# Performance work log

Hardware: AMD Instinct MI355X
Metric: run time of the kernel (lower is better)

The kernel has to match this reference:

```python
import jax, jax.numpy as jnp
import numpy as np

B, S, D = 2, 2048, 2048
H = 16
NOPE, ROPE, VDIM = 128, 64, 128
QKD = NOPE + ROPE  # 192
KV_RANK = 512
EPS = 1e-6
SCALE = QKD ** -0.5  # rope_factor <= 1.0 -> no mscale correction


def _rotate_half(x):
    h = x.shape[-1] // 2
    return jnp.concatenate([-x[..., h:], x[..., :h]], axis=-1)


def _rms_norm(x, w):
    var = jnp.mean(jnp.square(x), axis=-1, keepdims=True)
    return x * jax.lax.rsqrt(var + EPS) * w


def setup_inputs() -> dict:
    key = jax.random.key(0)
    ks = jax.random.split(key, 8)
    hidden_states = jax.random.normal(ks[0], (B, S, D), dtype=jnp.float32)
    cos = jax.random.uniform(ks[1], (S, ROPE), dtype=jnp.float32)
    sin = jax.random.uniform(ks[2], (S, ROPE), dtype=jnp.float32)
    # parameters (torch Linear stores [out, in]; keep same layout)
    wq_w = jax.random.normal(ks[3], (H * QKD, D), dtype=jnp.float32) * (D ** -0.5)
    wkv_a_w = jax.random.normal(ks[4], (KV_RANK + ROPE, D), dtype=jnp.float32) * (D ** -0.5)
    kv_norm_w = jnp.ones((KV_RANK,), dtype=jnp.float32)
    wkv_b_w = jax.random.normal(ks[5], (H * (NOPE + VDIM), KV_RANK), dtype=jnp.float32) * (KV_RANK ** -0.5)
    wo_w = jax.random.normal(ks[6], (D, H * VDIM), dtype=jnp.float32) * ((H * VDIM) ** -0.5)
    return dict(hidden_states=hidden_states, cos=cos, sin=sin,
                wq_w=wq_w, wkv_a_w=wkv_a_w, kv_norm_w=kv_norm_w,
                wkv_b_w=wkv_b_w, wo_w=wo_w)


def reference(hidden_states, cos, sin, wq_w, wkv_a_w, kv_norm_w, wkv_b_w, wo_w):
    x = hidden_states
    # q projection (q_lora_rank == 0 path)
    q = jnp.einsum('bsd,od->bso', x, wq_w).reshape(B, S, H, QKD)
    q_nope, q_pe = q[..., :NOPE], q[..., NOPE:]
    # low-rank kv
    kv_all = jnp.einsum('bsd,od->bso', x, wkv_a_w)  # [B,S,KV_RANK+ROPE]
    kv, k_pe = kv_all[..., :KV_RANK], kv_all[..., KV_RANK:]
    kv_proj = jnp.einsum('bsr,or->bso', _rms_norm(kv, kv_norm_w), wkv_b_w)
    kv_proj = kv_proj.reshape(B, S, H, NOPE + VDIM)
    k_nope, v = kv_proj[..., :NOPE], kv_proj[..., NOPE:]
    # rotary on pe parts; k_pe broadcast over heads
    c = cos[None, :, None, :]  # [1,S,1,ROPE]
    s = sin[None, :, None, :]
    q_pe = q_pe * c + _rotate_half(q_pe) * s
    k_pe_h = k_pe[:, :, None, :]  # broadcast over heads
    k_pe_h = k_pe_h * c + _rotate_half(k_pe_h) * s
    k_pe_h = jnp.broadcast_to(k_pe_h, (B, S, H, ROPE))
    k = jnp.concatenate([k_nope, k_pe_h], axis=-1)  # [B,S,H,QKD]
    qf = jnp.concatenate([q_nope, q_pe], axis=-1)
    # naive attention, fp32 softmax
    scores = jnp.einsum('bshd,bthd->bsht', qf, k) * SCALE
    attn = jax.nn.softmax(scores.astype(jnp.float32), axis=-1).astype(x.dtype)
    out = jnp.einsum('bsht,bthd->bshd', attn, v).reshape(B, S, H * VDIM)
    return jnp.einsum('bsf,of->bso', out, wo_w)
```

## Files before the change

kernel.cpp:

```cpp
#include <hip/hip_runtime.h>
#include <cstdint>


typedef _Float16 f16;
typedef _Float16 f16x8 __attribute__((ext_vector_type(8)));
typedef _Float16 f16x4 __attribute__((ext_vector_type(4)));
typedef float    f32x4 __attribute__((ext_vector_type(4)));

#define SCALE 0.07216878364870322f

__device__ __forceinline__ void gl2lds16(const void* g, void* lds_wave_base) {
  __builtin_amdgcn_global_load_lds(
      (const __attribute__((address_space(1))) uint32_t*)(uintptr_t)g,
      (__attribute__((address_space(3))) uint32_t*)(uint32_t)(uintptr_t)lds_wave_base,
      16, 0, 0);
}

__global__ __launch_bounds__(256) void k_cvt(
    const float* __restrict__ x, const float* __restrict__ wq,
    const float* __restrict__ wkvb, const float* __restrict__ wo,
    const float* __restrict__ wkva,
    f16* __restrict__ xb, f16* __restrict__ wqb,
    f16* __restrict__ wkvbb, f16* __restrict__ wob,
    f16* __restrict__ wkvab)
{
  size_t i = ((size_t)blockIdx.x * 256 + threadIdx.x) * 4;
  if (i >= 20971520ull) {
    size_t il = i - 20971520ull;
    int r = (int)(il >> 11);
    f16x4 h;
    if (r < 576) {
      float4 v = *(const float4*)(wkva + il);
      h[0]=(f16)v.x; h[1]=(f16)v.y; h[2]=(f16)v.z; h[3]=(f16)v.w;
    } else { h[0]=h[1]=h[2]=h[3]=(f16)0.f; }
    *(f16x4*)(wkvab + il) = h;
    return;
  }
  const float* src; f16* dst; size_t off; float scl = 1.0f;
  if (i < 8388608ull)            { src = x;    dst = xb;    off = i; }
  else if (i < 14680064ull)      { src = wq;   dst = wqb;   off = i - 8388608ull; scl = SCALE; }
  else if (i < 16777216ull)      { src = wkvb; dst = wkvbb; off = i - 14680064ull; }
  else                           { src = wo;   dst = wob;   off = i - 16777216ull; }
  float4 v = *(const float4*)(src + off);
  f16x4 h; h[0]=(f16)(v.x*scl); h[1]=(f16)(v.y*scl); h[2]=(f16)(v.z*scl); h[3]=(f16)(v.w*scl);
  *(f16x4*)(dst + off) = h;
}

template<class Epi>
__device__ __forceinline__ void gemm_core(const f16* __restrict__ Ablk,
                                          const f16* __restrict__ Bblk,
                                          int K, Epi epi)
{
  __shared__ __align__(16) f16 As[128 * 64];
  __shared__ __align__(16) f16 Bs[128 * 64];

  const int tid  = threadIdx.x;
  const int lane = tid & 63;
  const int wv   = tid >> 6;
  const int wm = (wv >> 1) * 64, wn = (wv & 1) * 64;
  const int lrow = lane & 15;
  const int lk   = lane >> 4;

  f32x4 acc[4][4];
#pragma unroll
  for (int i = 0; i < 4; ++i)
#pragma unroll
    for (int j = 0; j < 4; ++j) acc[i][j] = f32x4{0.f, 0.f, 0.f, 0.f};

  for (int k0 = 0; k0 < K; k0 += 64) {
    __syncthreads();
#pragma unroll
    for (int it = 0; it < 4; ++it) {
      int s  = it * 256 + tid;
      int r  = s >> 3, sc = s & 7;
      int gc = sc ^ (r & 7);
      gl2lds16(Ablk + (size_t)r * K + k0 + gc * 8, (f16*)As + (size_t)(it * 256 + wv * 64) * 8);
      gl2lds16(Bblk + (size_t)r * K + k0 + gc * 8, (f16*)Bs + (size_t)(it * 256 + wv * 64) * 8);
    }
    __syncthreads();

#pragma unroll
    for (int ks = 0; ks < 2; ++ks) {
      f16x8 af[4], bf[4];
#pragma unroll
      for (int i = 0; i < 4; ++i) {
        int ra = wm + i * 16 + lrow;
        int ca = (ks * 4 + lk) ^ (ra & 7);
        af[i] = *(const f16x8*)(As + ra * 64 + ca * 8);
        int rb = wn + i * 16 + lrow;
        int cb = (ks * 4 + lk) ^ (rb & 7);
        bf[i] = *(const f16x8*)(Bs + rb * 64 + cb * 8);
      }
#pragma unroll
      for (int i = 0; i < 4; ++i)
#pragma unroll
        for (int j = 0; j < 4; ++j)
          acc[i][j] = __builtin_amdgcn_mfma_f32_16x16x32_f16(af[i], bf[j], acc[i][j], 0, 0, 0);
    }
  }
  epi(acc, wm, wn, lk, lrow);
}

__global__ __launch_bounds__(256, 3) void k_gemm_qkva(
    const f16* __restrict__ xb, const f16* __restrict__ wqb,
    const f16* __restrict__ wkvab, const float* __restrict__ cosb,
    const float* __restrict__ sinb,
    f16* __restrict__ qraw, f16* __restrict__ kva)
{
  int nb = blockIdx.x, m0 = blockIdx.y * 128;
  bool isq = nb < 24;
  const f16* Bblk; f16* Cb; int ldc;
  if (isq) { Bblk = wqb + (size_t)nb * 128 * 2048;
             Cb = qraw + (size_t)m0 * 3072 + nb * 128; ldc = 3072; }
  else     { int n0 = (nb - 24) * 128;
             Bblk = wkvab + (size_t)n0 * 2048;
             Cb = kva + (size_t)m0 * 640 + n0; ldc = 640; }
  gemm_core(xb + (size_t)m0 * 2048, Bblk, 2048,
    [&](f32x4 (&acc)[4][4], int wm, int wn, int lk, int lrow) {
      if (isq && (((nb << 1) + (wn >> 6)) % 3) == 2) {
#pragma unroll
        for (int i = 0; i < 4; ++i)
#pragma unroll
          for (int rr = 0; rr < 4; ++rr) {
            int row = wm + i * 16 + lk * 4 + rr;
            int s = (m0 + row) & 2047;
            const float* cbp = cosb + (size_t)s * 64;
            const float* sbp = sinb + (size_t)s * 64;
#pragma unroll
            for (int j = 0; j < 4; ++j) {
              int t = j * 16 + lrow;
              float v  = acc[i][j][rr];
              float pr = acc[i][j ^ 2][rr];
              float o = (j < 2) ? (v * cbp[t] - pr * sbp[t])
                                : (v * cbp[t] + pr * sbp[t]);
              Cb[(size_t)row * ldc + wn + j * 16 + lrow] = (f16)o;
            }
          }
        return;
      }
#pragma unroll
      for (int i = 0; i < 4; ++i)
#pragma unroll
        for (int rr = 0; rr < 4; ++rr) {
          int row = wm + i * 16 + lk * 4 + rr;
#pragma unroll
          for (int j = 0; j < 4; ++j)
            Cb[(size_t)row * ldc + wn + j * 16 + lrow] = (f16)acc[i][j][rr];
        }
    });
}

__global__ __launch_bounds__(256, 3) void k_gemm_kvb(
    const f16* __restrict__ kvn, const f16* __restrict__ wkvbb,
    f16* __restrict__ knope, f16* __restrict__ vf)
{
  int nb = blockIdx.x, m0 = blockIdx.y * 128;
  int hh = nb >> 1;
  bool isv = nb & 1;
  gemm_core(kvn + (size_t)m0 * 512, wkvbb + (size_t)nb * 128 * 512, 512,
    [&](f32x4 (&acc)[4][4], int wm, int wn, int lk, int lrow) {
      if (isv) {
#pragma unroll
        for (int i = 0; i < 4; ++i)
#pragma unroll
          for (int j = 0; j < 4; ++j) {
            int vd = wn + j * 16 + lrow;
            int trow = m0 + wm + i * 16 + lk * 4;
            int bb = trow >> 11, ss = trow & 2047;
            f16x4 pk;
#pragma unroll
            for (int rr = 0; rr < 4; ++rr) pk[rr] = (f16)acc[i][j][rr];
            *(f16x4*)(vf + ((size_t)(bb * 16 + hh) * 128 + vd) * 2048 + ss) = pk;
          }
      } else {
#pragma unroll
        for (int i = 0; i < 4; ++i)
#pragma unroll
          for (int rr = 0; rr < 4; ++rr) {
            int trow = m0 + wm + i * 16 + lk * 4 + rr;
#pragma unroll
            for (int j = 0; j < 4; ++j)
              knope[(size_t)trow * 2048 + hh * 128 + wn + j * 16 + lrow] = (f16)acc[i][j][rr];
          }
      }
    });
}

__global__ __launch_bounds__(256, 3) void k_gemm_out(
    const f16* __restrict__ aout, const f16* __restrict__ wob, float* __restrict__ out)
{
  int n0 = blockIdx.x * 128, m0 = blockIdx.y * 128;
  gemm_core(aout + (size_t)m0 * 2048, wob + (size_t)n0 * 2048, 2048,
    [&](f32x4 (&acc)[4][4], int wm, int wn, int lk, int lrow) {
#pragma unroll
      for (int i = 0; i < 4; ++i)
#pragma unroll
        for (int rr = 0; rr < 4; ++rr) {
          int row = m0 + wm + i * 16 + lk * 4 + rr;
#pragma unroll
          for (int j = 0; j < 4; ++j)
            out[(size_t)row * 2048 + n0 + wn + j * 16 + lrow] = acc[i][j][rr];
        }
    });
}

__global__ __launch_bounds__(256) void k_rmsnorm_rope(
    const f16* __restrict__ kva, const float* __restrict__ w,
    const float* __restrict__ cosb, const float* __restrict__ sinb,
    f16* __restrict__ kvn, f16* __restrict__ kper)
{
  int row = blockIdx.x;
  int s = row & 2047;
  const f16* in = kva + (size_t)row * 640;
  int t = threadIdx.x;
  float v0 = (float)in[t], v1 = (float)in[t + 256];
  float ss = v0 * v0 + v1 * v1;
#pragma unroll
  for (int m = 1; m < 64; m <<= 1) ss += __shfl_xor(ss, m);
  __shared__ float red[4];
  if ((t & 63) == 0) red[t >> 6] = ss;
  __syncthreads();
  float tot = red[0] + red[1] + red[2] + red[3];
  float sc = rsqrtf(tot * (1.0f / 512.0f) + 1e-6f);
  kvn[(size_t)row * 512 + t]       = (f16)(v0 * sc * w[t]);
  kvn[(size_t)row * 512 + t + 256] = (f16)(v1 * sc * w[t + 256]);
  if (t < 32) {
    float a = (float)in[512 + t], bq = (float)in[512 + t + 32];
    float c0 = cosb[s * 64 + t], s0 = sinb[s * 64 + t];
    float c1 = cosb[s * 64 + t + 32], s1 = sinb[s * 64 + t + 32];
    kper[(size_t)row * 64 + t]      = (f16)(a * c0 - bq * s0);
    kper[(size_t)row * 64 + t + 32] = (f16)(bq * c1 + a * s1);
  }
}

#define PSTR 84

__global__ __launch_bounds__(512, 2) void k_attn(
    const f16* __restrict__ qraw, const f16* __restrict__ knope,
    const f16* __restrict__ kper, const f16* __restrict__ vf,
    f16* __restrict__ aout)
{
  int linear = blockIdx.x;
  int xcd  = linear & 7;
  int slot = linear >> 3;
  int hb   = (xcd << 2) | (slot & 3);
  int qt   = slot >> 2;
  int h = hb & 15, b = hb >> 4;
  int q0 = qt * 256;
  int tid = threadIdx.x, lane = tid & 63, wv = tid >> 6;
  int lrow = lane & 15, lk = lane >> 4;

  __shared__ __align__(16) f16 Ks[2][64 * 192];
  __shared__ __align__(16) f16 Vs[2][128 * 64];
  __shared__ __align__(16) f16 Ps[8][32 * PSTR];

  f16x8 qfr[2][6];
#pragma unroll
  for (int m = 0; m < 2; ++m) {
    const f16* qb = qraw + ((size_t)(b * 2048 + q0 + wv * 32 + m * 16 + lrow)) * 3072
                    + h * 192 + lk * 8;
#pragma unroll
    for (int ks = 0; ks < 6; ++ks) qfr[m][ks] = *(const f16x8*)(qb + ks * 32);
  }

  f32x4 oacc[2][8];
#pragma unroll
  for (int m = 0; m < 2; ++m)
#pragma unroll
    for (int i = 0; i < 8; ++i) oacc[m][i] = f32x4{0.f, 0.f, 0.f, 0.f};
  float l_st[2][4];
#pragma unroll
  for (int m = 0; m < 2; ++m)
#pragma unroll
    for (int r = 0; r < 4; ++r) l_st[m][r] = 0.f;

  const f16* knb = knope + ((size_t)b * 2048) * 2048 + h * 128;
  const f16* kpb = kper + (size_t)b * 2048 * 64;
  const f16* vb_ = vf + ((size_t)(b * 16 + h)) * 128 * 2048;

  const char* kp_ptr[3]; int kp_step[3];
#pragma unroll
  for (int it = 0; it < 3; ++it) {
    int s = it * 512 + tid;
    int r = s / 24, c = s - r * 24;
    int gc = c ^ (r & 7);
    if (gc < 16) { kp_ptr[it] = (const char*)(knb + (size_t)r * 2048 + gc * 8); kp_step[it] = 64 * 2048 * 2; }
    else         { kp_ptr[it] = (const char*)(kpb + (size_t)r * 64 + (gc - 16) * 8); kp_step[it] = 64 * 64 * 2; }
  }
  const char* vp_ptr[2];
#pragma unroll
  for (int it = 0; it < 2; ++it) {
    int s = it * 512 + tid;
    int r = s >> 3, c = s & 7, gc = c ^ (r & 7);
    vp_ptr[it] = (const char*)(vb_ + (size_t)r * 2048 + gc * 8);
  }

#pragma unroll
  for (int it = 0; it < 3; ++it) {
    gl2lds16(kp_ptr[it], (f16*)Ks[0] + (size_t)(it * 512 + wv * 64) * 8);
    kp_ptr[it] += kp_step[it];
  }
#pragma unroll
  for (int it = 0; it < 2; ++it) {
    gl2lds16(vp_ptr[it], (f16*)Vs[0] + (size_t)(it * 512 + wv * 64) * 8);
    vp_ptr[it] += 64 * 2;
  }

  int cur = 0;
  for (int t0 = 0; t0 < 2048; t0 += 64) {
    __syncthreads();
    if (t0 + 64 < 2048) {
#pragma unroll
      for (int it = 0; it < 3; ++it) {
        gl2lds16(kp_ptr[it], (f16*)Ks[cur ^ 1] + (size_t)(it * 512 + wv * 64) * 8);
        kp_ptr[it] += kp_step[it];
      }
#pragma unroll
      for (int it = 0; it < 2; ++it) {
        gl2lds16(vp_ptr[it], (f16*)Vs[cur ^ 1] + (size_t)(it * 512 + wv * 64) * 8);
        vp_ptr[it] += 64 * 2;
      }
    }
    const f16* Kc = Ks[cur];
    const f16* Vc = Vs[cur];

    f32x4 sacc[2][4];
#pragma unroll
    for (int m = 0; m < 2; ++m)
#pragma unroll
      for (int nt = 0; nt < 4; ++nt) sacc[m][nt] = f32x4{0.f, 0.f, 0.f, 0.f};
    __builtin_amdgcn_s_setprio(1);
#pragma unroll
    for (int nt = 0; nt < 4; ++nt) {
      int rb = nt * 16 + lrow;
#pragma unroll
      for (int ks = 0; ks < 6; ++ks) {
        int cc = (ks * 4 + lk) ^ (rb & 7);
        f16x8 bfr = *(const f16x8*)(Kc + rb * 192 + cc * 8);
        sacc[0][nt] = __builtin_amdgcn_mfma_f32_16x16x32_f16(qfr[0][ks], bfr, sacc[0][nt], 0, 0, 0);
        sacc[1][nt] = __builtin_amdgcn_mfma_f32_16x16x32_f16(qfr[1][ks], bfr, sacc[1][nt], 0, 0, 0);
      }
    }
    __builtin_amdgcn_s_setprio(0);

#pragma unroll
    for (int m = 0; m < 2; ++m) {
#pragma unroll
      for (int r = 0; r < 4; ++r) {
        float p0 = __expf(sacc[m][0][r]);
        float p1 = __expf(sacc[m][1][r]);
        float p2 = __expf(sacc[m][2][r]);
        float p3 = __expf(sacc[m][3][r]);
        l_st[m][r] += (p0 + p1) + (p2 + p3);
        int prow = (m * 16 + lk * 4 + r) * PSTR;
        Ps[wv][prow + 0 * 16 + lrow] = (f16)p0;
        Ps[wv][prow + 1 * 16 + lrow] = (f16)p1;
        Ps[wv][prow + 2 * 16 + lrow] = (f16)p2;
        Ps[wv][prow + 3 * 16 + lrow] = (f16)p3;
      }
    }
    __builtin_amdgcn_s_waitcnt(0xC07F);

    __builtin_amdgcn_s_setprio(1);
#pragma unroll
    for (int ks2 = 0; ks2 < 2; ++ks2) {
      f16x8 pa0 = *(const f16x8*)(&Ps[wv][(0 * 16 + lrow) * PSTR + ks2 * 32 + lk * 8]);
      f16x8 pa1 = *(const f16x8*)(&Ps[wv][(1 * 16 + lrow) * PSTR + ks2 * 32 + lk * 8]);
#pragma unroll
      for (int nv = 0; nv < 8; ++nv) {
        int rv = nv * 16 + lrow;
        int cc = (ks2 * 4 + lk) ^ (rv & 7);
        f16x8 vbf = *(const f16x8*)(Vc + rv * 64 + cc * 8);
        oacc[0][nv] = __builtin_amdgcn_mfma_f32_16x16x32_f16(pa0, vbf, oacc[0][nv], 0, 0, 0);
        oacc[1][nv] = __builtin_amdgcn_mfma_f32_16x16x32_f16(pa1, vbf, oacc[1][nv], 0, 0, 0);
      }
    }
    __builtin_amdgcn_s_setprio(0);
    cur ^= 1;
  }

  float rinv[2][4];
#pragma unroll
  for (int m = 0; m < 2; ++m)
#pragma unroll
    for (int r = 0; r < 4; ++r) {
      float l = l_st[m][r];
#pragma unroll
      for (int msk = 1; msk < 16; msk <<= 1) l += __shfl_xor(l, msk);
      rinv[m][r] = 1.0f / l;
    }
#pragma unroll
  for (int m = 0; m < 2; ++m) {
    f16* ob = aout + ((size_t)(b * 2048 + q0 + wv * 32 + m * 16 + lk * 4)) * 2048
              + h * 128 + lrow;
#pragma unroll
    for (int nv = 0; nv < 8; ++nv)
#pragma unroll
      for (int rr = 0; rr < 4; ++rr)
        ob[(size_t)rr * 2048 + nv * 16] = (f16)(oacc[m][nv][rr] * rinv[m][rr]);
  }
}

extern "C" void kernel_launch(void* const* d_in, const int* in_sizes, int n_in,
                              void* d_out, int out_size, void* d_ws, size_t ws_size,
                              hipStream_t stream)
{
  const float* x    = (const float*)d_in[0];
  const float* cosb = (const float*)d_in[1];
  const float* sinb = (const float*)d_in[2];
  const float* wq   = (const float*)d_in[3];
  const float* wkva = (const float*)d_in[4];
  const float* knw  = (const float*)d_in[5];
  const float* wkvb = (const float*)d_in[6];
  const float* wo   = (const float*)d_in[7];
  float* out = (float*)d_out;

  char* p = (char*)d_ws;
  auto take = [&](size_t elems) { char* r = p; p += (elems * 2 + 255) & ~(size_t)255; return r; };
  f16* xb    = (f16*)take(8388608ull);
  f16* wqb   = (f16*)take(6291456ull);
  f16* wkvab = (f16*)take(1310720ull);
  f16* wkvbb = (f16*)take(2097152ull);
  f16* wob   = (f16*)take(4194304ull);
  f16* qraw  = (f16*)take(12582912ull);
  f16* kva   = (f16*)take(2621440ull);
  f16* kvn   = (f16*)take(2097152ull);
  f16* kper  = (f16*)take(262144ull);
  f16* knope = (f16*)take(8388608ull);
  f16* vf    = (f16*)take(8388608ull);
  f16* aout  = (f16*)take(8388608ull);

  k_cvt<<<21760, 256, 0, stream>>>(x, wq, wkvb, wo, wkva, xb, wqb, wkvbb, wob, wkvab);
  k_gemm_qkva<<<dim3(29, 32), 256, 0, stream>>>(xb, wqb, wkvab, cosb, sinb, qraw, kva);
  k_rmsnorm_rope<<<4096, 256, 0, stream>>>(kva, knw, cosb, sinb, kvn, kper);
  k_gemm_kvb<<<dim3(32, 32), 256, 0, stream>>>(kvn, wkvbb, knope, vf);
  k_attn<<<dim3(256), 512, 0, stream>>>(qraw, knope, kper, vf, aout);
  k_gemm_out<<<dim3(16, 32), 256, 0, stream>>>(aout, wob, out);
}
```

Measured before the change: 389.9 us.

## Halve attention Q and KV tiles, double the grid, fold log2e into Q scale

The attention kernel now gives each wave 16 query rows instead of 32 and streams K/V in 32-key tiles instead of 64. This doubles the grid to 512 blocks and raises the launch-bounds occupancy target to 4 blocks per CU, trading register and LDS footprint for more resident waves to hide latency. The price is that each K/V tile is reused by half as many queries, so global and L2 traffic for K/V roughly doubles. Separately, log2(e) is folded into the Q weight scale at conversion so the softmax can use the hardware exp2 instead of __expf.

```diff
diff --git a/kernel.cpp b/kernel.cpp
--- a/kernel.cpp
+++ b/kernel.cpp
@@ -7,7 +7,7 @@
 typedef _Float16 f16x4 __attribute__((ext_vector_type(4)));
 typedef float    f32x4 __attribute__((ext_vector_type(4)));
 
-#define SCALE 0.07216878364870322f
+#define SCALE_L2E 0.104117550f
 
 __device__ __forceinline__ void gl2lds16(const void* g, void* lds_wave_base) {
   __builtin_amdgcn_global_load_lds(
@@ -38,7 +38,7 @@
   }
   const float* src; f16* dst; size_t off; float scl = 1.0f;
   if (i < 8388608ull)            { src = x;    dst = xb;    off = i; }
-  else if (i < 14680064ull)      { src = wq;   dst = wqb;   off = i - 8388608ull; scl = SCALE; }
+  else if (i < 14680064ull)      { src = wq;   dst = wqb;   off = i - 8388608ull; scl = SCALE_L2E; }
   else if (i < 16777216ull)      { src = wkvb; dst = wkvbb; off = i - 14680064ull; }
   else                           { src = wo;   dst = wob;   off = i - 16777216ull; }
   float4 v = *(const float4*)(src + off);
@@ -233,9 +233,9 @@
   }
 }
 
-#define PSTR 84
-
-__global__ __launch_bounds__(512, 2) void k_attn(
+#define PSTR 42
+
+__global__ __launch_bounds__(512, 4) void k_attn(
     const f16* __restrict__ qraw, const f16* __restrict__ knope,
     const f16* __restrict__ kper, const f16* __restrict__ vf,
     f16* __restrict__ aout)
@@ -246,159 +246,125 @@
   int hb   = (xcd << 2) | (slot & 3);
   int qt   = slot >> 2;
   int h = hb & 15, b = hb >> 4;
-  int q0 = qt * 256;
+  int q0 = qt * 128;
   int tid = threadIdx.x, lane = tid & 63, wv = tid >> 6;
   int lrow = lane & 15, lk = lane >> 4;
 
-  __shared__ __align__(16) f16 Ks[2][64 * 192];
-  __shared__ __align__(16) f16 Vs[2][128 * 64];
-  __shared__ __align__(16) f16 Ps[8][32 * PSTR];
-
-  f16x8 qfr[2][6];
-#pragma unroll
-  for (int m = 0; m < 2; ++m) {
-    const f16* qb = qraw + ((size_t)(b * 2048 + q0 + wv * 32 + m * 16 + lrow)) * 3072
+  __shared__ __align__(16) f16 Ks[2][32 * 192];
+  __shared__ __align__(16) f16 Vs[2][128 * 32];
+  __shared__ __align__(16) f16 Ps[8][16 * PSTR];
+
+  f16x8 qfr[6];
+  {
+    const f16* qb = qraw + ((size_t)(b * 2048 + q0 + wv * 16 + lrow)) * 3072
                     + h * 192 + lk * 8;
 #pragma unroll
-    for (int ks = 0; ks < 6; ++ks) qfr[m][ks] = *(const f16x8*)(qb + ks * 32);
-  }
-
-  f32x4 oacc[2][8];
-#pragma unroll
-  for (int m = 0; m < 2; ++m)
-#pragma unroll
-    for (int i = 0; i < 8; ++i) oacc[m][i] = f32x4{0.f, 0.f, 0.f, 0.f};
-  float l_st[2][4];
-#pragma unroll
-  for (int m = 0; m < 2; ++m)
-#pragma unroll
-    for (int r = 0; r < 4; ++r) l_st[m][r] = 0.f;
+    for (int ks = 0; ks < 6; ++ks) qfr[ks] = *(const f16x8*)(qb + ks * 32);
+  }
+
+  f32x4 oacc[8];
+#pragma unroll
+  for (int i = 0; i < 8; ++i) oacc[i] = f32x4{0.f, 0.f, 0.f, 0.f};
+  float l_st[4];
+#pragma unroll
+  for (int r = 0; r < 4; ++r) l_st[r] = 0.f;
 
   const f16* knb = knope + ((size_t)b * 2048) * 2048 + h * 128;
   const f16* kpb = kper + (size_t)b * 2048 * 64;
   const f16* vb_ = vf + ((size_t)(b * 16 + h)) * 128 * 2048;
 
-  const char* kp_ptr[3]; int kp_step[3];
-#pragma unroll
-  for (int it = 0; it < 3; ++it) {
+  const char* kp_ptr[2]; int kp_step[2];
+#pragma unroll
+  for (int it = 0; it < 2; ++it) {
     int s = it * 512 + tid;
     int r = s / 24, c = s - r * 24;
     int gc = c ^ (r & 7);
-    if (gc < 16) { kp_ptr[it] = (const char*)(knb + (size_t)r * 2048 + gc * 8); kp_step[it] = 64 * 2048 * 2; }
-    else         { kp_ptr[it] = (const char*)(kpb + (size_t)r * 64 + (gc - 16) * 8); kp_step[it] = 64 * 64 * 2; }
-  }
-  const char* vp_ptr[2];
-#pragma unroll
-  for (int it = 0; it < 2; ++it) {
-    int s = it * 512 + tid;
-    int r = s >> 3, c = s & 7, gc = c ^ (r & 7);
-    vp_ptr[it] = (const char*)(vb_ + (size_t)r * 2048 + gc * 8);
-  }
-
-#pragma unroll
-  for (int it = 0; it < 3; ++it) {
-    gl2lds16(kp_ptr[it], (f16*)Ks[0] + (size_t)(it * 512 + wv * 64) * 8);
-    kp_ptr[it] += kp_step[it];
-  }
-#pragma unroll
-  for (int it = 0; it < 2; ++it) {
-    gl2lds16(vp_ptr[it], (f16*)Vs[0] + (size_t)(it * 512 + wv * 64) * 8);
-    vp_ptr[it] += 64 * 2;
-  }
+    if (gc < 16) { kp_ptr[it] = (const char*)(knb + (size_t)r * 2048 + gc * 8); kp_step[it] = 32 * 2048 * 2; }
+    else         { kp_ptr[it] = (const char*)(kpb + (size_t)r * 64 + (gc - 16) * 8); kp_step[it] = 32 * 64 * 2; }
+  }
+  const char* vp_ptr;
+  {
+    int r = tid >> 2, c = tid & 3;
+    int gc = c ^ ((r ^ (r >> 2)) & 3);
+    vp_ptr = (const char*)(vb_ + (size_t)r * 2048 + gc * 8);
+  }
+
+  gl2lds16(kp_ptr[0], (f16*)Ks[0] + (size_t)(wv * 64) * 8);
+  kp_ptr[0] += kp_step[0];
+  if (wv < 4) gl2lds16(kp_ptr[1], (f16*)Ks[0] + (size_t)(512 + wv * 64) * 8);
+  kp_ptr[1] += kp_step[1];
+  gl2lds16(vp_ptr, (f16*)Vs[0] + (size_t)(wv * 64) * 8);
+  vp_ptr += 32 * 2;
 
   int cur = 0;
-  for (int t0 = 0; t0 < 2048; t0 += 64) {
+  for (int t0 = 0; t0 < 2048; t0 += 32) {
     __syncthreads();
-    if (t0 + 64 < 2048) {
-#pragma unroll
-      for (int it = 0; it < 3; ++it) {
-        gl2lds16(kp_ptr[it], (f16*)Ks[cur ^ 1] + (size_t)(it * 512 + wv * 64) * 8);
-        kp_ptr[it] += kp_step[it];
-      }
-#pragma unroll
-      for (int it = 0; it < 2; ++it) {
-        gl2lds16(vp_ptr[it], (f16*)Vs[cur ^ 1] + (size_t)(it * 512 + wv * 64) * 8);
-        vp_ptr[it] += 64 * 2;
-      }
+    if (t0 + 32 < 2048) {
+      gl2lds16(kp_ptr[0], (f16*)Ks[cur ^ 1] + (size_t)(wv * 64) * 8);
+      kp_ptr[0] += kp_step[0];
+      if (wv < 4) gl2lds16(kp_ptr[1], (f16*)Ks[cur ^ 1] + (size_t)(512 + wv * 64) * 8);
+      kp_ptr[1] += kp_step[1];
+      gl2lds16(vp_ptr, (f16*)Vs[cur ^ 1] + (size_t)(wv * 64) * 8);
+      vp_ptr += 32 * 2;
     }
     const f16* Kc = Ks[cur];
     const f16* Vc = Vs[cur];
 
-    f32x4 sacc[2][4];
-#pragma unroll
-    for (int m = 0; m < 2; ++m)
-#pragma unroll
-      for (int nt = 0; nt < 4; ++nt) sacc[m][nt] = f32x4{0.f, 0.f, 0.f, 0.f};
+    f32x4 sacc[2];
+    sacc[0] = f32x4{0.f, 0.f, 0.f, 0.f};
+    sacc[1] = f32x4{0.f, 0.f, 0.f, 0.f};
     __builtin_amdgcn_s_setprio(1);
 #pragma unroll
-    for (int nt = 0; nt < 4; ++nt) {
+    for (int nt = 0; nt < 2; ++nt) {
       int rb = nt * 16 + lrow;
 #pragma unroll
       for (int ks = 0; ks < 6; ++ks) {
         int cc = (ks * 4 + lk) ^ (rb & 7);
         f16x8 bfr = *(const f16x8*)(Kc + rb * 192 + cc * 8);
-        sacc[0][nt] = __builtin_amdgcn_mfma_f32_16x16x32_f16(qfr[0][ks], bfr, sacc[0][nt], 0, 0, 0);
-        sacc[1][nt] = __builtin_amdgcn_mfma_f32_16x16x32_f16(qfr[1][ks], bfr, sacc[1][nt], 0, 0, 0);
+        sacc[nt] = __builtin_amdgcn_mfma_f32_16x16x32_f16(qfr[ks], bfr, sacc[nt], 0, 0, 0);
       }
     }
     __builtin_amdgcn_s_setprio(0);
 
 #pragma unroll
-    for (int m = 0; m < 2; ++m) {
-#pragma unroll
-      for (int r = 0; r < 4; ++r) {
-        float p0 = __expf(sacc[m][0][r]);
-        float p1 = __expf(sacc[m][1][r]);
-        float p2 = __expf(sacc[m][2][r]);
-        float p3 = __expf(sacc[m][3][r]);
-        l_st[m][r] += (p0 + p1) + (p2 + p3);
-        int prow = (m * 16 + lk * 4 + r) * PSTR;
-        Ps[wv][prow + 0 * 16 + lrow] = (f16)p0;
-        Ps[wv][prow + 1 * 16 + lrow] = (f16)p1;
-        Ps[wv][prow + 2 * 16 + lrow] = (f16)p2;
-        Ps[wv][prow + 3 * 16 + lrow] = (f16)p3;
-      }
+    for (int r = 0; r < 4; ++r) {
+      float p0 = __builtin_amdgcn_exp2f(sacc[0][r]);
+      float p1 = __builtin_amdgcn_exp2f(sacc[1][r]);
+      l_st[r] += p0 + p1;
+      int prow = (lk * 4 + r) * PSTR;
+      Ps[wv][prow + lrow]      = (f16)p0;
+      Ps[wv][prow + 16 + lrow] = (f16)p1;
     }
     __builtin_amdgcn_s_waitcnt(0xC07F);
 
     __builtin_amdgcn_s_setprio(1);
-#pragma unroll
-    for (int ks2 = 0; ks2 < 2; ++ks2) {
-      f16x8 pa0 = *(const f16x8*)(&Ps[wv][(0 * 16 + lrow) * PSTR + ks2 * 32 + lk * 8]);
-      f16x8 pa1 = *(const f16x8*)(&Ps[wv][(1 * 16 + lrow) * PSTR + ks2 * 32 + lk * 8]);
-#pragma unroll
-      for (int nv = 0; nv < 8; ++nv) {
-        int rv = nv * 16 + lrow;
-        int cc = (ks2 * 4 + lk) ^ (rv & 7);
-        f16x8 vbf = *(const f16x8*)(Vc + rv * 64 + cc * 8);
-        oacc[0][nv] = __builtin_amdgcn_mfma_f32_16x16x32_f16(pa0, vbf, oacc[0][nv], 0, 0, 0);
-        oacc[1][nv] = __builtin_amdgcn_mfma_f32_16x16x32_f16(pa1, vbf, oacc[1][nv], 0, 0, 0);
-      }
+    f16x8 pa = *(const f16x8*)(&Ps[wv][lrow * PSTR + lk * 8]);
+#pragma unroll
+    for (int nv = 0; nv < 8; ++nv) {
+      int rv = nv * 16 + lrow;
+      int cc = lk ^ ((rv ^ (rv >> 2)) & 3);
+      f16x8 vbf = *(const f16x8*)(Vc + rv * 32 + cc * 8);
+      oacc[nv] = __builtin_amdgcn_mfma_f32_16x16x32_f16(pa, vbf, oacc[nv], 0, 0, 0);
     }
     __builtin_amdgcn_s_setprio(0);
     cur ^= 1;
   }
 
-  float rinv[2][4];
-#pragma unroll
-  for (int m = 0; m < 2; ++m)
-#pragma unroll
-    for (int r = 0; r < 4; ++r) {
-      float l = l_st[m][r];
-#pragma unroll
-      for (int msk = 1; msk < 16; msk <<= 1) l += __shfl_xor(l, msk);
-      rinv[m][r] = 1.0f / l;
-    }
-#pragma unroll
-  for (int m = 0; m < 2; ++m) {
-    f16* ob = aout + ((size_t)(b * 2048 + q0 + wv * 32 + m * 16 + lk * 4)) * 2048
-              + h * 128 + lrow;
-#pragma unroll
-    for (int nv = 0; nv < 8; ++nv)
-#pragma unroll
-      for (int rr = 0; rr < 4; ++rr)
-        ob[(size_t)rr * 2048 + nv * 16] = (f16)(oacc[m][nv][rr] * rinv[m][rr]);
-  }
+  float rinv[4];
+#pragma unroll
+  for (int r = 0; r < 4; ++r) {
+    float l = l_st[r];
+#pragma unroll
+    for (int msk = 1; msk < 16; msk <<= 1) l += __shfl_xor(l, msk);
+    rinv[r] = 1.0f / l;
+  }
+  f16* ob = aout + ((size_t)(b * 2048 + q0 + wv * 16 + lk * 4)) * 2048
+            + h * 128 + lrow;
+#pragma unroll
+  for (int nv = 0; nv < 8; ++nv)
+#pragma unroll
+    for (int rr = 0; rr < 4; ++rr)
+      ob[(size_t)rr * 2048 + nv * 16] = (f16)(oacc[nv][rr] * rinv[rr]);
 }
 
 extern "C" void kernel_launch(void* const* d_in, const int* in_sizes, int n_in,
@@ -434,6 +400,6 @@
   k_gemm_qkva<<<dim3(29, 32), 256, 0, stream>>>(xb, wqb, wkvab, cosb, sinb, qraw, kva);
   k_rmsnorm_rope<<<4096, 256, 0, stream>>>(kva, knw, cosb, sinb, kvn, kper);
   k_gemm_kvb<<<dim3(32, 32), 256, 0, stream>>>(kvn, wkvbb, knope, vf);
-  k_attn<<<dim3(256), 512, 0, stream>>>(qraw, knope, kper, vf, aout);
+  k_attn<<<dim3(512), 512, 0, stream>>>(qraw, knope, kper, vf, aout);
   k_gemm_out<<<dim3(16, 32), 256, 0, stream>>>(aout, wob, out);
 }
```

After: 385.5 us. No clear change (-1.1%).

## Use 256x256 double-buffered GEMM tiles and fold log2e into Q scale

Applied to the files above, without the earlier changes.

Adds a 256x256 tile GEMM core with 512 threads and double-buffered LDS, prefetching the next K-tile while MFMAs run. The QKV-A and KV-B projections move to this core, which raises data reuse per block and cuts the number of blocks. The softmax scale now includes log2(e), so attention can use the native exp2 instead of expf. Risks: the grids get smaller (240 and 256 blocks), so load balance across CUs is worse; the 128 KB of LDS limits occupancy; and the padded wkva rows add wasted work.

```diff
diff --git a/kernel.cpp b/kernel.cpp
--- a/kernel.cpp
+++ b/kernel.cpp
@@ -7,7 +7,7 @@
 typedef _Float16 f16x4 __attribute__((ext_vector_type(4)));
 typedef float    f32x4 __attribute__((ext_vector_type(4)));
 
-#define SCALE 0.07216878364870322f
+#define SCALE_L2E 0.104117550f
 
 __device__ __forceinline__ void gl2lds16(const void* g, void* lds_wave_base) {
   __builtin_amdgcn_global_load_lds(
@@ -38,12 +38,202 @@
   }
   const float* src; f16* dst; size_t off; float scl = 1.0f;
   if (i < 8388608ull)            { src = x;    dst = xb;    off = i; }
-  else if (i < 14680064ull)      { src = wq;   dst = wqb;   off = i - 8388608ull; scl = SCALE; }
+  else if (i < 14680064ull)      { src = wq;   dst = wqb;   off = i - 8388608ull; scl = SCALE_L2E; }
   else if (i < 16777216ull)      { src = wkvb; dst = wkvbb; off = i - 14680064ull; }
   else                           { src = wo;   dst = wob;   off = i - 16777216ull; }
   float4 v = *(const float4*)(src + off);
   f16x4 h; h[0]=(f16)(v.x*scl); h[1]=(f16)(v.y*scl); h[2]=(f16)(v.z*scl); h[3]=(f16)(v.w*scl);
   *(f16x4*)(dst + off) = h;
+}
+
+template<class Epi>
+__device__ __forceinline__ void gemm256_core(const f16* __restrict__ Ablk,
+                                             const f16* __restrict__ Bblk,
+                                             int K, Epi epi)
+{
+  __shared__ __align__(16) f16 As[2][256 * 64];
+  __shared__ __align__(16) f16 Bs[2][256 * 64];
+
+  const int tid  = threadIdx.x;
+  const int lane = tid & 63;
+  const int wv   = tid >> 6;
+  const int wm   = (wv >> 2) * 128;
+  const int wn   = (wv & 3) * 64;
+  const int lrow = lane & 15;
+  const int lk   = lane >> 4;
+
+  f32x4 acc[8][4];
+#pragma unroll
+  for (int i = 0; i < 8; ++i)
+#pragma unroll
+    for (int j = 0; j < 4; ++j) acc[i][j] = f32x4{0.f, 0.f, 0.f, 0.f};
+
+  const int NT = K >> 6;
+
+  const f16* aptr[4]; const f16* bptr[4]; int ldsbase[4];
+#pragma unroll
+  for (int q = 0; q < 4; ++q) {
+    int s = q * 512 + tid;
+    int r = s >> 3, c = s & 7;
+    int gc = c ^ (r & 7);
+    aptr[q] = Ablk + (size_t)r * K + gc * 8;
+    bptr[q] = Bblk + (size_t)r * K + gc * 8;
+    ldsbase[q] = (q * 512 + wv * 64) * 8;
+  }
+
+#pragma unroll
+  for (int q = 0; q < 4; ++q) gl2lds16(aptr[q], (f16*)As[0] + ldsbase[q]);
+#pragma unroll
+  for (int q = 0; q < 4; ++q) gl2lds16(bptr[q], (f16*)Bs[0] + ldsbase[q]);
+
+  for (int t = 0; t < NT; ++t) {
+    const int cur = t & 1;
+    asm volatile("s_waitcnt vmcnt(0)" ::: "memory");
+    __builtin_amdgcn_s_barrier();
+    asm volatile("" ::: "memory");
+    const f16* Ac = As[cur];
+    const f16* Bc = Bs[cur];
+    const bool more = (t + 1 < NT);
+    const int koff = (t + 1) * 64;
+#pragma unroll
+    for (int p = 0; p < 4; ++p) {
+      if (p == 0 && more) {
+#pragma unroll
+        for (int q = 0; q < 4; ++q)
+          gl2lds16(aptr[q] + koff, (f16*)As[cur ^ 1] + ldsbase[q]);
+      }
+      if (p == 1 && more) {
+#pragma unroll
+        for (int q = 0; q < 4; ++q)
+          gl2lds16(bptr[q] + koff, (f16*)Bs[cur ^ 1] + ldsbase[q]);
+      }
+      const int mh = p >> 1, nh = p & 1;
+      f16x8 af[2][4], bf[2][2];
+#pragma unroll
+      for (int ks = 0; ks < 2; ++ks) {
+#pragma unroll
+        for (int i = 0; i < 4; ++i) {
+          int ra = wm + mh * 64 + i * 16 + lrow;
+          int ca = (ks * 4 + lk) ^ (ra & 7);
+          af[ks][i] = *(const f16x8*)(Ac + ra * 64 + ca * 8);
+        }
+#pragma unroll
+        for (int j = 0; j < 2; ++j) {
+          int rb = wn + nh * 32 + j * 16 + lrow;
+          int cb = (ks * 4 + lk) ^ (rb & 7);
+          bf[ks][j] = *(const f16x8*)(Bc + rb * 64 + cb * 8);
+        }
+      }
+      __builtin_amdgcn_s_setprio(1);
+#pragma unroll
+      for (int ks = 0; ks < 2; ++ks)
+#pragma unroll
+        for (int i = 0; i < 4; ++i)
+#pragma unroll
+          for (int j = 0; j < 2; ++j)
+            acc[mh * 4 + i][nh * 2 + j] = __builtin_amdgcn_mfma_f32_16x16x32_f16(
+                af[ks][i], bf[ks][j], acc[mh * 4 + i][nh * 2 + j], 0, 0, 0);
+      __builtin_amdgcn_s_setprio(0);
+    }
+  }
+  epi(acc, wm, wn, lk, lrow);
+}
+
+__global__ __launch_bounds__(512, 2) void k_gemm_qkva(
+    const f16* __restrict__ xb, const f16* __restrict__ wqb,
+    const f16* __restrict__ wkvab, const float* __restrict__ cosb,
+    const float* __restrict__ sinb,
+    f16* __restrict__ qraw, f16* __restrict__ kva)
+{
+  int nb = blockIdx.x, m0 = blockIdx.y * 256;
+  bool isq = nb < 12;
+  const f16* Bblk = isq ? wqb + (size_t)nb * 256 * 2048
+                        : wkvab + (size_t)(nb - 12) * 256 * 2048;
+  gemm256_core(xb + (size_t)m0 * 2048, Bblk, 2048,
+    [&](f32x4 (&acc)[8][4], int wm, int wn, int lk, int lrow) {
+      if (isq) {
+        f16* Cb = qraw + (size_t)m0 * 3072 + nb * 256;
+        int g = nb * 4 + (wn >> 6);
+        if (g % 3 == 2) {
+#pragma unroll
+          for (int I = 0; I < 8; ++I)
+#pragma unroll
+            for (int rr = 0; rr < 4; ++rr) {
+              int row = wm + I * 16 + lk * 4 + rr;
+              int s = (m0 + row) & 2047;
+              const float* cbp = cosb + (size_t)s * 64;
+              const float* sbp = sinb + (size_t)s * 64;
+#pragma unroll
+              for (int J = 0; J < 4; ++J) {
+                int tt = J * 16 + lrow;
+                float v  = acc[I][J][rr];
+                float pr = acc[I][J ^ 2][rr];
+                float o = (J < 2) ? (v * cbp[tt] - pr * sbp[tt])
+                                  : (v * cbp[tt] + pr * sbp[tt]);
+                Cb[(size_t)row * 3072 + wn + J * 16 + lrow] = (f16)o;
+              }
+            }
+          return;
+        }
+#pragma unroll
+        for (int I = 0; I < 8; ++I)
+#pragma unroll
+          for (int rr = 0; rr < 4; ++rr) {
+            int row = wm + I * 16 + lk * 4 + rr;
+#pragma unroll
+            for (int J = 0; J < 4; ++J)
+              Cb[(size_t)row * 3072 + wn + J * 16 + lrow] = (f16)acc[I][J][rr];
+          }
+      } else {
+        int n0k = (nb - 12) * 256;
+        if (n0k + wn >= 640) return;
+        f16* Cb = kva + (size_t)m0 * 640 + n0k;
+#pragma unroll
+        for (int I = 0; I < 8; ++I)
+#pragma unroll
+          for (int rr = 0; rr < 4; ++rr) {
+            int row = wm + I * 16 + lk * 4 + rr;
+#pragma unroll
+            for (int J = 0; J < 4; ++J)
+              Cb[(size_t)row * 640 + wn + J * 16 + lrow] = (f16)acc[I][J][rr];
+          }
+      }
+    });
+}
+
+__global__ __launch_bounds__(512, 2) void k_gemm_kvb(
+    const f16* __restrict__ kvn, const f16* __restrict__ wkvbb,
+    f16* __restrict__ knope, f16* __restrict__ vf)
+{
+  int hh = blockIdx.x, m0 = blockIdx.y * 256;
+  gemm256_core(kvn + (size_t)m0 * 512, wkvbb + (size_t)hh * 256 * 512, 512,
+    [&](f32x4 (&acc)[8][4], int wm, int wn, int lk, int lrow) {
+      if (wn >= 128) {
+#pragma unroll
+        for (int I = 0; I < 8; ++I) {
+          int trow = m0 + wm + I * 16 + lk * 4;
+          int bb = trow >> 11, ss = trow & 2047;
+#pragma unroll
+          for (int J = 0; J < 4; ++J) {
+            int vd = (wn - 128) + J * 16 + lrow;
+            f16x4 pk;
+#pragma unroll
+            for (int rr = 0; rr < 4; ++rr) pk[rr] = (f16)acc[I][J][rr];
+            *(f16x4*)(vf + ((size_t)(bb * 16 + hh) * 128 + vd) * 2048 + ss) = pk;
+          }
+        }
+      } else {
+#pragma unroll
+        for (int I = 0; I < 8; ++I)
+#pragma unroll
+          for (int rr = 0; rr < 4; ++rr) {
+            int trow = m0 + wm + I * 16 + lk * 4 + rr;
+#pragma unroll
+            for (int J = 0; J < 4; ++J)
+              knope[(size_t)trow * 2048 + hh * 128 + wn + J * 16 + lrow] = (f16)acc[I][J][rr];
+          }
+      }
+    });
 }
 
 template<class Epi>
@@ -99,91 +289,6 @@
     }
   }
   epi(acc, wm, wn, lk, lrow);
-}
-
-__global__ __launch_bounds__(256, 3) void k_gemm_qkva(
-    const f16* __restrict__ xb, const f16* __restrict__ wqb,
-    const f16* __restrict__ wkvab, const float* __restrict__ cosb,
-    const float* __restrict__ sinb,
-    f16* __restrict__ qraw, f16* __restrict__ kva)
-{
-  int nb = blockIdx.x, m0 = blockIdx.y * 128;
-  bool isq = nb < 24;
-  const f16* Bblk; f16* Cb; int ldc;
-  if (isq) { Bblk = wqb + (size_t)nb * 128 * 2048;
-             Cb = qraw + (size_t)m0 * 3072 + nb * 128; ldc = 3072; }
-  else     { int n0 = (nb - 24) * 128;
-             Bblk = wkvab + (size_t)n0 * 2048;
-             Cb = kva + (size_t)m0 * 640 + n0; ldc = 640; }
-  gemm_core(xb + (size_t)m0 * 2048, Bblk, 2048,
-    [&](f32x4 (&acc)[4][4], int wm, int wn, int lk, int lrow) {
-      if (isq && (((nb << 1) + (wn >> 6)) % 3) == 2) {
-#pragma unroll
-        for (int i = 0; i < 4; ++i)
-#pragma unroll
-          for (int rr = 0; rr < 4; ++rr) {
-            int row = wm + i * 16 + lk * 4 + rr;
-            int s = (m0 + row) & 2047;
-            const float* cbp = cosb + (size_t)s * 64;
-            const float* sbp = sinb + (size_t)s * 64;
-#pragma unroll
-            for (int j = 0; j < 4; ++j) {
-              int t = j * 16 + lrow;
-              float v  = acc[i][j][rr];
-              float pr = acc[i][j ^ 2][rr];
-              float o = (j < 2) ? (v * cbp[t] - pr * sbp[t])
-                                : (v * cbp[t] + pr * sbp[t]);
-              Cb[(size_t)row * ldc + wn + j * 16 + lrow] = (f16)o;
-            }
-          }
-        return;
-      }
-#pragma unroll
-      for (int i = 0; i < 4; ++i)
-#pragma unroll
-        for (int rr = 0; rr < 4; ++rr) {
-          int row = wm + i * 16 + lk * 4 + rr;
-#pragma unroll
-          for (int j = 0; j < 4; ++j)
-            Cb[(size_t)row * ldc + wn + j * 16 + lrow] = (f16)acc[i][j][rr];
-        }
-    });
-}
-
-__global__ __launch_bounds__(256, 3) void k_gemm_kvb(
-    const f16* __restrict__ kvn, const f16* __restrict__ wkvbb,
-    f16* __restrict__ knope, f16* __restrict__ vf)
-{
-  int nb = blockIdx.x, m0 = blockIdx.y * 128;
-  int hh = nb >> 1;
-  bool isv = nb & 1;
-  gemm_core(kvn + (size_t)m0 * 512, wkvbb + (size_t)nb * 128 * 512, 512,
-    [&](f32x4 (&acc)[4][4], int wm, int wn, int lk, int lrow) {
-      if (isv) {
-#pragma unroll
-        for (int i = 0; i < 4; ++i)
-#pragma unroll
-          for (int j = 0; j < 4; ++j) {
-            int vd = wn + j * 16 + lrow;
-            int trow = m0 + wm + i * 16 + lk * 4;
-            int bb = trow >> 11, ss = trow & 2047;
-            f16x4 pk;
-#pragma unroll
-            for (int rr = 0; rr < 4; ++rr) pk[rr] = (f16)acc[i][j][rr];
-            *(f16x4*)(vf + ((size_t)(bb * 16 + hh) * 128 + vd) * 2048 + ss) = pk;
-          }
-      } else {
-#pragma unroll
-        for (int i = 0; i < 4; ++i)
-#pragma unroll
-          for (int rr = 0; rr < 4; ++rr) {
-            int trow = m0 + wm + i * 16 + lk * 4 + rr;
-#pragma unroll
-            for (int j = 0; j < 4; ++j)
-              knope[(size_t)trow * 2048 + hh * 128 + wn + j * 16 + lrow] = (f16)acc[i][j][rr];
-          }
-      }
-    });
 }
 
 __global__ __launch_bounds__(256, 3) void k_gemm_out(
@@ -347,10 +452,10 @@
     for (int m = 0; m < 2; ++m) {
 #pragma unroll
       for (int r = 0; r < 4; ++r) {
-        float p0 = __expf(sacc[m][0][r]);
-        float p1 = __expf(sacc[m][1][r]);
-        float p2 = __expf(sacc[m][2][r]);
-        float p3 = __expf(sacc[m][3][r]);
+        float p0 = __builtin_amdgcn_exp2f(sacc[m][0][r]);
+        float p1 = __builtin_amdgcn_exp2f(sacc[m][1][r]);
+        float p2 = __builtin_amdgcn_exp2f(sacc[m][2][r]);
+        float p3 = __builtin_amdgcn_exp2f(sacc[m][3][r]);
         l_st[m][r] += (p0 + p1) + (p2 + p3);
         int prow = (m * 16 + lk * 4 + r) * PSTR;
         Ps[wv][prow + 0 * 16 + lrow] = (f16)p0;
@@ -419,7 +524,7 @@
   auto take = [&](size_t elems) { char* r = p; p += (elems * 2 + 255) & ~(size_t)255; return r; };
   f16* xb    = (f16*)take(8388608ull);
   f16* wqb   = (f16*)take(6291456ull);
-  f16* wkvab = (f16*)take(1310720ull);
+  f16* wkvab = (f16*)take(1572864ull);
   f16* wkvbb = (f16*)take(2097152ull);
   f16* wob   = (f16*)take(4194304ull);
   f16* qraw  = (f16*)take(12582912ull);
@@ -430,10 +535,10 @@
   f16* vf    = (f16*)take(8388608ull);
   f16* aout  = (f16*)take(8388608ull);
 
-  k_cvt<<<21760, 256, 0, stream>>>(x, wq, wkvb, wo, wkva, xb, wqb, wkvbb, wob, wkvab);
-  k_gemm_qkva<<<dim3(29, 32), 256, 0, stream>>>(xb, wqb, wkvab, cosb, sinb, qraw, kva);
+  k_cvt<<<22016, 256, 0, stream>>>(x, wq, wkvb, wo, wkva, xb, wqb, wkvbb, wob, wkvab);
+  k_gemm_qkva<<<dim3(15, 16), 512, 0, stream>>>(xb, wqb, wkvab, cosb, sinb, qraw, kva);
   k_rmsnorm_rope<<<4096, 256, 0, stream>>>(kva, knw, cosb, sinb, kvn, kper);
-  k_gemm_kvb<<<dim3(32, 32), 256, 0, stream>>>(kvn, wkvbb, knope, vf);
+  k_gemm_kvb<<<dim3(16, 16), 512, 0, stream>>>(kvn, wkvbb, knope, vf);
   k_attn<<<dim3(256), 512, 0, stream>>>(qraw, knope, kper, vf, aout);
   k_gemm_out<<<dim3(16, 32), 256, 0, stream>>>(aout, wob, out);
 }
```

New measurement: 373.4 us. -4.2%, faster.
